# Performance work log

Hardware: AMD Instinct MI355X
Metric: run time of the kernel (lower is better)

The kernel has to match this reference:

```python
import jax, jax.numpy as jnp
import numpy as np

# Module hyperparameters (init_kwargs)
KH, KW = 1, 1            # kernel_size
PATCH_H, PATCH_W = 21, 21  # patch_size (displacement grid)
SH, SW = 1, 1            # stride
PAD_H, PAD_W = 0, 0      # padding
DILP_H, DILP_W = 1, 1    # dilation_patch
B, C, H, W = 8, 256, 64, 96


def setup_inputs() -> dict:
    key = jax.random.key(0)
    k1, k2 = jax.random.split(key)
    input1 = jax.random.normal(k1, (B, C, H, W), dtype=jnp.float32)
    input2 = jax.random.normal(k2, (B, C, H, W), dtype=jnp.float32)
    return {"input1": input1, "input2": input2}


def _correlation(x1, x2):
    """FlowNet-style spatial correlation (cost volume).

    out[b, pi, pj, i, j] = sum_{c, ki, kj}
        x1_pad[b, c, i*SH + ki, j*SW + kj] *
        x2_pad[b, c, i*SH + ki + (pi - radH)*DILP_H, j*SW + kj + (pj - radW)*DILP_W]
    Out-of-bounds reads of x2 are zero (handled by padding).
    """
    radH, radW = PATCH_H // 2, PATCH_W // 2
    x1p = jnp.pad(x1, ((0, 0), (0, 0), (PAD_H, PAD_H), (PAD_W, PAD_W)))
    x2p = jnp.pad(x2, ((0, 0), (0, 0),
                       (PAD_H + radH * DILP_H, PAD_H + radH * DILP_H),
                       (PAD_W + radW * DILP_W, PAD_W + radW * DILP_W)))
    Hp, Wp = H + 2 * PAD_H, W + 2 * PAD_W
    oH = (Hp - KH) // SH + 1
    oW = (Wp - KW) // SW + 1

    # displacement grid -> start offsets into x2p (0 corresponds to -rad shift)
    sh = jnp.arange(PATCH_H, dtype=jnp.int32) * DILP_H
    sw = jnp.arange(PATCH_W, dtype=jnp.int32) * DILP_W
    starts = jnp.stack(jnp.meshgrid(sh, sw, indexing="ij"), axis=-1).reshape(-1, 2)

    def step(carry, s):
        # shifted view of x2 aligned with padded x1
        sl = jax.lax.dynamic_slice(x2p, (0, 0, s[0], s[1]), (B, C, Hp, Wp))
        prod = jnp.sum(x1p * sl, axis=1)  # [B, Hp, Wp], channel reduction
        # kernel-window sum + output stride (KH=KW=1 -> single strided slice)
        acc = jnp.zeros((B, oH, oW), dtype=prod.dtype)
        for ki in range(KH):
            for kj in range(KW):
                acc = acc + jax.lax.slice(
                    prod, (0, ki, kj),
                    (B, ki + (oH - 1) * SH + 1, kj + (oW - 1) * SW + 1),
                    (1, SH, SW))
        return carry, acc

    _, out = jax.lax.scan(step, None, starts)  # [PATCH_H*PATCH_W, B, oH, oW]
    out = out.reshape(PATCH_H, PATCH_W, B, oH, oW)
    return jnp.transpose(out, (2, 0, 1, 3, 4))  # [B, patchH, patchW, oH, oW]


def reference(input1, input2):
    return _correlation(input1, input2)
```

## Files before the change

kernel.cpp:

```cpp
#include <hip/hip_runtime.h>

typedef __attribute__((ext_vector_type(8))) short short8;
typedef __attribute__((ext_vector_type(4))) float f32x4;
typedef __attribute__((ext_vector_type(4))) unsigned short us4;

constexpr int NB = 8, NC = 256, IH = 64, IW = 96;
constexpr int PATCH = 21, RAD = 10;
constexpr int WIN = 28;
constexpr int KC = 32, NKS = NC / KC;
constexpr int PLANE = IH * IW;
constexpr int PH = IH + 2 * RAD, PW = IW + 2 * RAD;
constexpr int NPOS = 512;
constexpr int NBCH = NPOS * 4;
constexpr int NACH = 512;
constexpr int NCHUNK = NBCH + NACH;
constexpr int ASTR = IH * IW * KC;
constexpr int BSTR = PH * PW * KC;
constexpr size_t X1T_ELEMS = (size_t)NB * NKS * ASTR;
constexpr size_t X2P_ELEMS = (size_t)NB * NKS * BSTR;
constexpr int GSTR = 129;

__device__ __forceinline__ unsigned short f2bf(float f) {
  unsigned u = __builtin_bit_cast(unsigned, f);
  u += 0x7fffu + ((u >> 16) & 1u);
  return (unsigned short)(u >> 16);
}

__global__ __launch_bounds__(256) void x1_to_kmajor(
    const float* __restrict__ src, unsigned short* __restrict__ dst) {
  __shared__ float lsf[32 * 97];
  const int blk = blockIdx.x;
  const int ct = blk & 7, i = (blk >> 3) & 63, b = blk >> 9;
  const int c0 = ct * 32, t = threadIdx.x;
  const float* sp = src + ((size_t)b * NC + c0) * PLANE + (size_t)i * IW;
#pragma unroll
  for (int k = 0; k < 12; ++k) {
    int idx = k * 256 + t;
    int c = idx / 96, j = idx - c * 96;
    lsf[c * 97 + j] = sp[(size_t)c * PLANE + j];
  }
  __syncthreads();
  unsigned short* dp = dst + (((size_t)(b * NKS + ct) * IH + i) * IW) * KC;
#pragma unroll
  for (int k = 0; k < 3; ++k) {
    int o = k * 256 + t;
    int j = o >> 3, cq = o & 7;
    us4 v = {f2bf(lsf[(cq * 4 + 0) * 97 + j]), f2bf(lsf[(cq * 4 + 1) * 97 + j]),
             f2bf(lsf[(cq * 4 + 2) * 97 + j]), f2bf(lsf[(cq * 4 + 3) * 97 + j])};
    *(us4*)&dp[(size_t)j * KC + cq * 4] = v;
  }
}

__global__ __launch_bounds__(256) void x2_to_kmajor_pad(
    const float* __restrict__ src, unsigned short* __restrict__ dst) {
  __shared__ float lsf[32 * 97];
  const int blk = blockIdx.x;
  const int ct = blk & 7, i = (blk >> 3) % PH, b = blk / (PH * 8);
  const int c0 = ct * 32, t = threadIdx.x;
  const int isrc = i - RAD;
  const bool rowok = (unsigned)isrc < (unsigned)IH;
  if (rowok) {
    const float* sp = src + ((size_t)b * NC + c0) * PLANE + (size_t)isrc * IW;
#pragma unroll
    for (int k = 0; k < 12; ++k) {
      int idx = k * 256 + t;
      int c = idx / 96, j = idx - c * 96;
      lsf[c * 97 + j] = sp[(size_t)c * PLANE + j];
    }
  }
  __syncthreads();
  unsigned short* dp = dst + (((size_t)(b * NKS + ct) * PH + i) * PW) * KC;
#pragma unroll
  for (int k = 0; k < 4; ++k) {
    int o = k * 256 + t;
    if (o < PW * 8) {
      int j = o >> 3, cq = o & 7;
      int jsrc = j - RAD;
      us4 v = {0, 0, 0, 0};
      if (rowok && (unsigned)jsrc < (unsigned)IW)
        v = us4{f2bf(lsf[(cq * 4 + 0) * 97 + jsrc]), f2bf(lsf[(cq * 4 + 1) * 97 + jsrc]),
                f2bf(lsf[(cq * 4 + 2) * 97 + jsrc]), f2bf(lsf[(cq * 4 + 3) * 97 + jsrc])};
      *(us4*)&dp[(size_t)j * KC + cq * 4] = v;
    }
  }
}

__global__ __launch_bounds__(512, 2) void corr_half(
    const unsigned short* __restrict__ x1k, const unsigned short* __restrict__ x2k,
    float* __restrict__ out) {
  __shared__ __attribute__((aligned(16))) unsigned short ls[3 * NCHUNK * 8];

  const int t = threadIdx.x, lane = t & 63, wv = t >> 6;
  const int bid = blockIdx.x;
  const int b = bid & 7;
  const int tile = bid >> 3;
  const int v = tile & 1;
  const int tt = tile >> 1;
  const int ti = tt / 12, tj = tt % 12;
  const int i0 = 16 * ti, j0 = 8 * tj;
  const int mg = wv >> 2;
  const int cg = wv & 3;
  const int cbeg = 8 * cg;
  const int qk = lane >> 4, lr = lane & 15;

  const unsigned short* x1b = x1k + (size_t)b * NKS * ASTR;
  const unsigned short* x2b = x2k + (size_t)b * NKS * BSTR;

  const unsigned short* srcp[5];
#pragma unroll
  for (int it = 0; it < 5; ++it) {
    int q = it * 512 + t;
    if (q < NBCH) {
      int w = ((q >> 3) << 1) | (((q >> 2) ^ (q >> 4)) & 1);
      int c4 = (q & 3) ^ (w & 3);
      int wd = (w >= 504) ? (w - 504) : w;
      int wi = wd / WIN, wj = wd - wi * WIN;
      srcp[it] = x2b + ((size_t)(i0 + 18 * v + wi) * PW + (j0 + wj)) * KC + c4 * 8;
    } else {
      int qa = q - NBCH;
      int m = ((qa >> 3) << 1) | (((qa >> 2) ^ (qa >> 4)) & 1);
      int c4 = (qa & 3) ^ (m & 3);
      srcp[it] = x1b + ((size_t)(i0 + (m >> 3)) * IW + (j0 + (m & 7))) * KC + c4 * 8;
    }
  }

  f32x4 acc[4][8];
#pragma unroll
  for (int a = 0; a < 4; ++a)
#pragma unroll
    for (int cc = 0; cc < 8; ++cc) acc[a][cc] = (f32x4){0.f, 0.f, 0.f, 0.f};

#define STAGE(BUF, KS)                                                              \
  {                                                                                 \
    unsigned short* lb = &ls[(BUF) * NCHUNK * 8];                                   \
    _Pragma("unroll")                                                               \
    for (int it = 0; it < 5; ++it)                                                  \
      __builtin_amdgcn_global_load_lds(                                             \
          (const void*)(srcp[it] + (size_t)(KS) * (it < 4 ? BSTR : ASTR)),          \
          (void*)(lb + (it * 512 + wv * 64) * 8), 16, 0, 0);                        \
  }

#define COMPUTE(BUF)                                                                \
  {                                                                                 \
    const unsigned short* lb = &ls[(BUF) * NCHUNK * 8];                             \
    short8 af0 = *(const short8*)(lb + (NBCH + ((64 * (4 * mg + 0) + 4 * lr + qk) ^ (lr & 7))) * 8); \
    short8 af1 = *(const short8*)(lb + (NBCH + ((64 * (4 * mg + 1) + 4 * lr + qk) ^ (lr & 7))) * 8); \
    short8 af2 = *(const short8*)(lb + (NBCH + ((64 * (4 * mg + 2) + 4 * lr + qk) ^ (lr & 7))) * 8); \
    short8 af3 = *(const short8*)(lb + (NBCH + ((64 * (4 * mg + 3) + 4 * lr + qk) ^ (lr & 7))) * 8); \
    _Pragma("unroll")                                                               \
    for (int cc = 0; cc < 8; ++cc) {                                                \
      int wrow = 16 * (cbeg + cc) + lr;                                             \
      int slot = (4 * wrow + qk) ^ (lr & 7);                                        \
      short8 bf = *(const short8*)(lb + slot * 8);                                  \
      acc[0][cc] = __builtin_amdgcn_mfma_f32_16x16x32_bf16(af0, bf, acc[0][cc], 0, 0, 0); \
      acc[1][cc] = __builtin_amdgcn_mfma_f32_16x16x32_bf16(af1, bf, acc[1][cc], 0, 0, 0); \
      acc[2][cc] = __builtin_amdgcn_mfma_f32_16x16x32_bf16(af2, bf, acc[2][cc], 0, 0, 0); \
      acc[3][cc] = __builtin_amdgcn_mfma_f32_16x16x32_bf16(af3, bf, acc[3][cc], 0, 0, 0); \
    }                                                                               \
  }

  STAGE(0, 0)
  STAGE(1, 1)

#define ITER(KS, VM)                                           \
  if ((KS) < 6) STAGE(((KS) + 2) % 3, (KS) + 2)                \
  asm volatile("s_waitcnt vmcnt(" #VM ")" ::: "memory");       \
  asm volatile("s_barrier" ::: "memory");                      \
  COMPUTE((KS) % 3)                                            \
  asm volatile("s_barrier" ::: "memory");

  ITER(0, 10)
  ITER(1, 10)
  ITER(2, 10)
  ITER(3, 10)
  ITER(4, 10)
  ITER(5, 10)
  ITER(6, 5)
  ITER(7, 0)
#undef ITER
#undef COMPUTE
#undef STAGE

  float* gf = (float*)ls;
#pragma unroll
  for (int p = 0; p < 2 + 1; ++p) {
    __syncthreads();
    const int R0 = 168 * p;
#pragma unroll
    for (int a = 0; a < 4; ++a)
#pragma unroll
      for (int cc = 0; cc < 8; ++cc) {
        int n = 16 * (cbeg + cc) + lr;
        if (n >= R0 && n < R0 + 168) {
          int rl = n - R0;
          int sm = 4 * (4 * mg + a) + qk;
          float* gp = &gf[rl * GSTR + 4 * (sm ^ (rl & 7))];
          gp[0] = acc[a][cc][0]; gp[1] = acc[a][cc][1];
          gp[2] = acc[a][cc][2]; gp[3] = acc[a][cc][3];
        }
      }
    __syncthreads();
    int segs = 0;
#pragma unroll
    for (int kk = 0; kk < 6; ++kk) {
      int W = 18 * v + 6 * p + kk;
      int hi = W < 15 ? W : 15, lo = W - 20 > 0 ? W - 20 : 0;
      segs += hi - lo + 1;
    }
    segs *= 21;
    for (int s = t; s < segs; s += 512) {
      int pidx = s / 21, pj = s - pidx * 21;
      int k = 0, rem = pidx, stop = 0;
#pragma unroll
      for (int kk = 0; kk < 5; ++kk) {
        int W = 18 * v + 6 * p + kk;
        int hi = W < 15 ? W : 15, lo = W - 20 > 0 ? W - 20 : 0;
        int c = hi - lo + 1;
        int go = (!stop) && (rem >= c);
        rem -= go ? c : 0;
        k += go;
        stop |= !go;
      }
      int W = 18 * v + 6 * p + k;
      int lo = W - 20 > 0 ? W - 20 : 0;
      int ii = lo + rem;
      int pi = W - ii;
      int rl0 = 28 * k + pj;
      float g[8];
#pragma unroll
      for (int e = 0; e < 8; ++e) {
        int m = 8 * ii + e, row = rl0 + e;
        g[e] = gf[row * GSTR + 4 * ((m >> 2) ^ (row & 7)) + (m & 3)];
      }
      float* op = out + ((((size_t)b * PATCH + pi) * PATCH + pj) * IH + (i0 + ii)) * IW + j0;
      f32x4 v0 = {g[0], g[1], g[2], g[3]};
      f32x4 v1 = {g[4], g[5], g[6], g[7]};
      *(f32x4*)op = v0;
      *(f32x4*)(op + 4) = v1;
    }
  }
}

constexpr int LDKF = 40;
constexpr int NWINF = 784;
__global__ __launch_bounds__(512, 2) void corr_mfma_fb(
    const float* __restrict__ x1, const float* __restrict__ x2, float* __restrict__ out) {
  __shared__ __attribute__((aligned(16))) unsigned short lsA[64 * LDKF];
  __shared__ __attribute__((aligned(16))) unsigned short lsB[NWINF * LDKF];
  const int t = threadIdx.x;
  const int b = blockIdx.y;
  const int ti = blockIdx.x / 12, tj = blockIdx.x % 12;
  const int i0 = ti * 8, j0 = tj * 8;
  const int lane = t & 63, wv = t >> 6;
  const int mtp = wv >> 2, cg = wv & 3, cbeg = cg * 12;
  const int qk = lane >> 4, lr = lane & 15;
  f32x4 acc[2][13];
#pragma unroll
  for (int a = 0; a < 2; ++a)
#pragma unroll
    for (int cc = 0; cc < 13; ++cc) acc[a][cc] = (f32x4){0.f, 0.f, 0.f, 0.f};
  const int am = t & 63, ak4 = t >> 6;
  const int aii = am >> 3, ajj = am & 7;
  const float* x1p = x1 + ((size_t)b * NC + 4 * ak4) * PLANE + (size_t)(i0 + aii) * IW + (j0 + ajj);
  const float* x2b = x2 + (size_t)b * NC * PLANE;
  for (int ks = 0; ks < NKS; ++ks) {
    __syncthreads();
    {
      const float* p = x1p + (size_t)ks * KC * PLANE;
      us4 v = {f2bf(p[0]), f2bf(p[PLANE]), f2bf(p[2 * PLANE]), f2bf(p[3 * PLANE])};
      *(us4*)&lsA[am * LDKF + 4 * ak4] = v;
    }
    for (int w = t; w < NWINF; w += 512) {
      const int wi = w / WIN, wj = w - wi * WIN;
      const int gi = i0 - RAD + wi, gj = j0 - RAD + wj;
      const bool ok = ((unsigned)gi < (unsigned)IH) && ((unsigned)gj < (unsigned)IW);
      const float* p = x2b + ((size_t)(ks * KC) * IH + gi) * IW + gj;
      unsigned short* dst = &lsB[w * LDKF];
#pragma unroll
      for (int k4 = 0; k4 < 8; ++k4) {
        const float* q = p + (size_t)(4 * k4) * PLANE;
        us4 v = {f2bf(ok ? q[0] : 0.f), f2bf(ok ? q[PLANE] : 0.f),
                 f2bf(ok ? q[2 * PLANE] : 0.f), f2bf(ok ? q[3 * PLANE] : 0.f)};
        *(us4*)&dst[4 * k4] = v;
      }
    }
    __syncthreads();
    short8 a0 = *(const short8*)&lsA[(32 * mtp + lr) * LDKF + 8 * qk];
    short8 a1 = *(const short8*)&lsA[(32 * mtp + 16 + lr) * LDKF + 8 * qk];
#pragma unroll
    for (int cc = 0; cc < 13; ++cc) {
      const int wrow = 16 * (cbeg + cc) + lr;
      short8 bf = *(const short8*)&lsB[wrow * LDKF + 8 * qk];
      acc[0][cc] = __builtin_amdgcn_mfma_f32_16x16x32_bf16(a0, bf, acc[0][cc], 0, 0, 0);
      acc[1][cc] = __builtin_amdgcn_mfma_f32_16x16x32_bf16(a1, bf, acc[1][cc], 0, 0, 0);
    }
  }
#pragma unroll
  for (int a = 0; a < 2; ++a) {
    const int mb = 16 * (2 * mtp + a) + qk * 4;
#pragma unroll
    for (int cc = 0; cc < 13; ++cc) {
      if (cg > 0 && cc == 0) continue;
      const int n = 16 * (cbeg + cc) + lr;
      const int wi = n / WIN, wj = n - wi * WIN;
#pragma unroll
      for (int r = 0; r < 4; ++r) {
        const int m = mb + r;
        const int ii = m >> 3, jj = m & 7;
        const int pi = wi - ii, pj = wj - jj;
        if ((unsigned)pi < (unsigned)PATCH && (unsigned)pj < (unsigned)PATCH)
          out[((((size_t)b * PATCH + pi) * PATCH + pj) * IH + (i0 + ii)) * IW + (j0 + jj)] =
              acc[a][cc][r];
      }
    }
  }
}

extern "C" void kernel_launch(void* const* d_in, const int* in_sizes, int n_in,
                              void* d_out, int out_size, void* d_ws, size_t ws_size,
                              hipStream_t stream) {
  const float* x1 = (const float*)d_in[0];
  const float* x2 = (const float*)d_in[1];
  float* out = (float*)d_out;
  const size_t need = (X1T_ELEMS + X2P_ELEMS) * sizeof(unsigned short);
  if (ws_size >= need) {
    unsigned short* x1k = (unsigned short*)d_ws;
    unsigned short* x2k = x1k + X1T_ELEMS;
    x1_to_kmajor<<<NB * IH * 8, 256, 0, stream>>>(x1, x1k);
    x2_to_kmajor_pad<<<NB * PH * 8, 256, 0, stream>>>(x2, x2k);
    corr_half<<<NB * 96, 512, 0, stream>>>(x1k, x2k, out);
  } else {
    dim3 grid(96, NB);
    corr_mfma_fb<<<grid, 512, 0, stream>>>(x1, x2, out);
  }
}
```

Measured before the change: 87.73 us.

## Merge layout prepasses into one launch and switch correlation to 32x32 MFMA

The two fp32-to-bf16 k-major conversion kernels are merged into a single launch, and their global reads are widened to float4. The main correlation kernel now uses 32x32x16 bf16 MFMA tiles instead of 16x16x32. Each wave holds 2x4 32x32 accumulators rather than the 4x8 16x16 grid, which changes the LDS fragment reads and the epilogue scatter layout. The goal is to cut launch overhead, reduce global load instructions, and raise MFMA efficiency with fewer LDS fragment loads. The cost is a different register footprint and an unswizzled epilogue write that may cause LDS bank conflicts.

```diff
diff --git a/kernel.cpp b/kernel.cpp
--- a/kernel.cpp
+++ b/kernel.cpp
@@ -2,6 +2,7 @@
 
 typedef __attribute__((ext_vector_type(8))) short short8;
 typedef __attribute__((ext_vector_type(4))) float f32x4;
+typedef __attribute__((ext_vector_type(16))) float f32x16;
 typedef __attribute__((ext_vector_type(4))) unsigned short us4;
 
 constexpr int NB = 8, NC = 256, IH = 64, IW = 96;
@@ -19,6 +20,8 @@
 constexpr size_t X1T_ELEMS = (size_t)NB * NKS * ASTR;
 constexpr size_t X2P_ELEMS = (size_t)NB * NKS * BSTR;
 constexpr int GSTR = 129;
+constexpr int X1BLKS = NB * IH * 8;
+constexpr int X2BLKS = NB * PH * 8;
 
 __device__ __forceinline__ unsigned short f2bf(float f) {
   unsigned u = __builtin_bit_cast(unsigned, f);
@@ -26,66 +29,70 @@
   return (unsigned short)(u >> 16);
 }
 
-__global__ __launch_bounds__(256) void x1_to_kmajor(
-    const float* __restrict__ src, unsigned short* __restrict__ dst) {
+__global__ __launch_bounds__(256) void prepass_kmajor(
+    const float* __restrict__ x1, const float* __restrict__ x2,
+    unsigned short* __restrict__ x1k, unsigned short* __restrict__ x2k) {
   __shared__ float lsf[32 * 97];
-  const int blk = blockIdx.x;
-  const int ct = blk & 7, i = (blk >> 3) & 63, b = blk >> 9;
-  const int c0 = ct * 32, t = threadIdx.x;
-  const float* sp = src + ((size_t)b * NC + c0) * PLANE + (size_t)i * IW;
-#pragma unroll
-  for (int k = 0; k < 12; ++k) {
-    int idx = k * 256 + t;
-    int c = idx / 96, j = idx - c * 96;
-    lsf[c * 97 + j] = sp[(size_t)c * PLANE + j];
-  }
-  __syncthreads();
-  unsigned short* dp = dst + (((size_t)(b * NKS + ct) * IH + i) * IW) * KC;
-#pragma unroll
-  for (int k = 0; k < 3; ++k) {
-    int o = k * 256 + t;
-    int j = o >> 3, cq = o & 7;
-    us4 v = {f2bf(lsf[(cq * 4 + 0) * 97 + j]), f2bf(lsf[(cq * 4 + 1) * 97 + j]),
-             f2bf(lsf[(cq * 4 + 2) * 97 + j]), f2bf(lsf[(cq * 4 + 3) * 97 + j])};
-    *(us4*)&dp[(size_t)j * KC + cq * 4] = v;
-  }
-}
-
-__global__ __launch_bounds__(256) void x2_to_kmajor_pad(
-    const float* __restrict__ src, unsigned short* __restrict__ dst) {
-  __shared__ float lsf[32 * 97];
-  const int blk = blockIdx.x;
-  const int ct = blk & 7, i = (blk >> 3) % PH, b = blk / (PH * 8);
-  const int c0 = ct * 32, t = threadIdx.x;
-  const int isrc = i - RAD;
-  const bool rowok = (unsigned)isrc < (unsigned)IH;
-  if (rowok) {
-    const float* sp = src + ((size_t)b * NC + c0) * PLANE + (size_t)isrc * IW;
-#pragma unroll
-    for (int k = 0; k < 12; ++k) {
+  const int t = threadIdx.x;
+  if (blockIdx.x < X1BLKS) {
+    const int blk = blockIdx.x;
+    const int ct = blk & 7, i = (blk >> 3) & 63, b = blk >> 9;
+    const int c0 = ct * 32;
+    const float* sp = x1 + ((size_t)b * NC + c0) * PLANE + (size_t)i * IW;
+#pragma unroll
+    for (int k = 0; k < 3; ++k) {
       int idx = k * 256 + t;
-      int c = idx / 96, j = idx - c * 96;
-      lsf[c * 97 + j] = sp[(size_t)c * PLANE + j];
-    }
-  }
-  __syncthreads();
-  unsigned short* dp = dst + (((size_t)(b * NKS + ct) * PH + i) * PW) * KC;
-#pragma unroll
-  for (int k = 0; k < 4; ++k) {
-    int o = k * 256 + t;
-    if (o < PW * 8) {
+      int c = idx / 24, j4 = idx - c * 24;
+      f32x4 v = *(const f32x4*)(sp + (size_t)c * PLANE + 4 * j4);
+      float* lp = &lsf[c * 97 + 4 * j4];
+      lp[0] = v[0]; lp[1] = v[1]; lp[2] = v[2]; lp[3] = v[3];
+    }
+    __syncthreads();
+    unsigned short* dp = x1k + (((size_t)(b * NKS + ct) * IH + i) * IW) * KC;
+#pragma unroll
+    for (int k = 0; k < 3; ++k) {
+      int o = k * 256 + t;
       int j = o >> 3, cq = o & 7;
-      int jsrc = j - RAD;
-      us4 v = {0, 0, 0, 0};
-      if (rowok && (unsigned)jsrc < (unsigned)IW)
-        v = us4{f2bf(lsf[(cq * 4 + 0) * 97 + jsrc]), f2bf(lsf[(cq * 4 + 1) * 97 + jsrc]),
-                f2bf(lsf[(cq * 4 + 2) * 97 + jsrc]), f2bf(lsf[(cq * 4 + 3) * 97 + jsrc])};
+      us4 v = {f2bf(lsf[(cq * 4 + 0) * 97 + j]), f2bf(lsf[(cq * 4 + 1) * 97 + j]),
+               f2bf(lsf[(cq * 4 + 2) * 97 + j]), f2bf(lsf[(cq * 4 + 3) * 97 + j])};
       *(us4*)&dp[(size_t)j * KC + cq * 4] = v;
     }
-  }
-}
-
-__global__ __launch_bounds__(512, 2) void corr_half(
+  } else {
+    const int blk = blockIdx.x - X1BLKS;
+    const int ct = blk & 7, i = (blk >> 3) % PH, b = blk / (PH * 8);
+    const int c0 = ct * 32;
+    const int isrc = i - RAD;
+    const bool rowok = (unsigned)isrc < (unsigned)IH;
+    if (rowok) {
+      const float* sp = x2 + ((size_t)b * NC + c0) * PLANE + (size_t)isrc * IW;
+#pragma unroll
+      for (int k = 0; k < 3; ++k) {
+        int idx = k * 256 + t;
+        int c = idx / 24, j4 = idx - c * 24;
+        f32x4 v = *(const f32x4*)(sp + (size_t)c * PLANE + 4 * j4);
+        float* lp = &lsf[c * 97 + 4 * j4];
+        lp[0] = v[0]; lp[1] = v[1]; lp[2] = v[2]; lp[3] = v[3];
+      }
+    }
+    __syncthreads();
+    unsigned short* dp = x2k + (((size_t)(b * NKS + ct) * PH + i) * PW) * KC;
+#pragma unroll
+    for (int k = 0; k < 4; ++k) {
+      int o = k * 256 + t;
+      if (o < PW * 8) {
+        int j = o >> 3, cq = o & 7;
+        int jsrc = j - RAD;
+        us4 v = {0, 0, 0, 0};
+        if (rowok && (unsigned)jsrc < (unsigned)IW)
+          v = us4{f2bf(lsf[(cq * 4 + 0) * 97 + jsrc]), f2bf(lsf[(cq * 4 + 1) * 97 + jsrc]),
+                  f2bf(lsf[(cq * 4 + 2) * 97 + jsrc]), f2bf(lsf[(cq * 4 + 3) * 97 + jsrc])};
+        *(us4*)&dp[(size_t)j * KC + cq * 4] = v;
+      }
+    }
+  }
+}
+
+__global__ __launch_bounds__(512, 2) void corr_half32(
     const unsigned short* __restrict__ x1k, const unsigned short* __restrict__ x2k,
     float* __restrict__ out) {
   __shared__ __attribute__((aligned(16))) unsigned short ls[3 * NCHUNK * 8];
@@ -98,9 +105,7 @@
   const int tt = tile >> 1;
   const int ti = tt / 12, tj = tt % 12;
   const int i0 = 16 * ti, j0 = 8 * tj;
-  const int mg = wv >> 2;
-  const int cg = wv & 3;
-  const int cbeg = 8 * cg;
+  const int l31 = lane & 31, h2 = lane >> 5;
   const int qk = lane >> 4, lr = lane & 15;
 
   const unsigned short* x1b = x1k + (size_t)b * NKS * ASTR;
@@ -123,12 +128,15 @@
       srcp[it] = x1b + ((size_t)(i0 + (m >> 3)) * IW + (j0 + (m & 7))) * KC + c4 * 8;
     }
   }
-
-  f32x4 acc[4][8];
-#pragma unroll
-  for (int a = 0; a < 4; ++a)
-#pragma unroll
-    for (int cc = 0; cc < 8; ++cc) acc[a][cc] = (f32x4){0.f, 0.f, 0.f, 0.f};
+  (void)qk; (void)lr;
+
+  f32x16 acc[2][4];
+#pragma unroll
+  for (int cc = 0; cc < 2; ++cc)
+#pragma unroll
+    for (int mt = 0; mt < 4; ++mt)
+#pragma unroll
+      for (int e = 0; e < 16; ++e) acc[cc][mt][e] = 0.f;
 
 #define STAGE(BUF, KS)                                                              \
   {                                                                                 \
@@ -143,19 +151,26 @@
 #define COMPUTE(BUF)                                                                \
   {                                                                                 \
     const unsigned short* lb = &ls[(BUF) * NCHUNK * 8];                             \
-    short8 af0 = *(const short8*)(lb + (NBCH + ((64 * (4 * mg + 0) + 4 * lr + qk) ^ (lr & 7))) * 8); \
-    short8 af1 = *(const short8*)(lb + (NBCH + ((64 * (4 * mg + 1) + 4 * lr + qk) ^ (lr & 7))) * 8); \
-    short8 af2 = *(const short8*)(lb + (NBCH + ((64 * (4 * mg + 2) + 4 * lr + qk) ^ (lr & 7))) * 8); \
-    short8 af3 = *(const short8*)(lb + (NBCH + ((64 * (4 * mg + 3) + 4 * lr + qk) ^ (lr & 7))) * 8); \
+    short8 afr[4][2];                                                               \
     _Pragma("unroll")                                                               \
-    for (int cc = 0; cc < 8; ++cc) {                                                \
-      int wrow = 16 * (cbeg + cc) + lr;                                             \
-      int slot = (4 * wrow + qk) ^ (lr & 7);                                        \
-      short8 bf = *(const short8*)(lb + slot * 8);                                  \
-      acc[0][cc] = __builtin_amdgcn_mfma_f32_16x16x32_bf16(af0, bf, acc[0][cc], 0, 0, 0); \
-      acc[1][cc] = __builtin_amdgcn_mfma_f32_16x16x32_bf16(af1, bf, acc[1][cc], 0, 0, 0); \
-      acc[2][cc] = __builtin_amdgcn_mfma_f32_16x16x32_bf16(af2, bf, acc[2][cc], 0, 0, 0); \
-      acc[3][cc] = __builtin_amdgcn_mfma_f32_16x16x32_bf16(af3, bf, acc[3][cc], 0, 0, 0); \
+    for (int mt = 0; mt < 4; ++mt)                                                  \
+      _Pragma("unroll")                                                             \
+      for (int h = 0; h < 2; ++h) {                                                 \
+        int m = 32 * mt + l31, c4q = 2 * h + h2;                                    \
+        afr[mt][h] = *(const short8*)(lb + (NBCH + ((4 * m + c4q) ^ (m & 7))) * 8); \
+      }                                                                             \
+    _Pragma("unroll")                                                               \
+    for (int cc = 0; cc < 2; ++cc) {                                                \
+      int wq = 32 * (2 * wv + cc) + l31;                                            \
+      _Pragma("unroll")                                                             \
+      for (int h = 0; h < 2; ++h) {                                                 \
+        int c4q = 2 * h + h2;                                                       \
+        short8 bf = *(const short8*)(lb + (((4 * wq + c4q) ^ (wq & 7))) * 8);       \
+        _Pragma("unroll")                                                           \
+        for (int mt = 0; mt < 4; ++mt)                                              \
+          acc[cc][mt] = __builtin_amdgcn_mfma_f32_32x32x16_bf16(afr[mt][h], bf,     \
+                                                                acc[cc][mt], 0, 0, 0); \
+      }                                                                             \
     }                                                                               \
   }
 
@@ -183,22 +198,26 @@
 
   float* gf = (float*)ls;
 #pragma unroll
-  for (int p = 0; p < 2 + 1; ++p) {
+  for (int p = 0; p < 3; ++p) {
     __syncthreads();
     const int R0 = 168 * p;
 #pragma unroll
-    for (int a = 0; a < 4; ++a)
-#pragma unroll
-      for (int cc = 0; cc < 8; ++cc) {
-        int n = 16 * (cbeg + cc) + lr;
-        if (n >= R0 && n < R0 + 168) {
-          int rl = n - R0;
-          int sm = 4 * (4 * mg + a) + qk;
-          float* gp = &gf[rl * GSTR + 4 * (sm ^ (rl & 7))];
-          gp[0] = acc[a][cc][0]; gp[1] = acc[a][cc][1];
-          gp[2] = acc[a][cc][2]; gp[3] = acc[a][cc][3];
-        }
-      }
+    for (int cc = 0; cc < 2; ++cc) {
+      int n = 32 * (2 * wv + cc) + l31;
+      if (n >= R0 && n < R0 + 168 && n < 504) {
+        float* gr = &gf[(n - R0) * GSTR];
+#pragma unroll
+        for (int mt = 0; mt < 4; ++mt)
+#pragma unroll
+          for (int q = 0; q < 4; ++q) {
+            float* gp = &gr[32 * mt + 8 * q + 4 * h2];
+            gp[0] = acc[cc][mt][4 * q + 0];
+            gp[1] = acc[cc][mt][4 * q + 1];
+            gp[2] = acc[cc][mt][4 * q + 2];
+            gp[3] = acc[cc][mt][4 * q + 3];
+          }
+      }
+    }
     __syncthreads();
     int segs = 0;
 #pragma unroll
@@ -228,10 +247,7 @@
       int rl0 = 28 * k + pj;
       float g[8];
 #pragma unroll
-      for (int e = 0; e < 8; ++e) {
-        int m = 8 * ii + e, row = rl0 + e;
-        g[e] = gf[row * GSTR + 4 * ((m >> 2) ^ (row & 7)) + (m & 3)];
-      }
+      for (int e = 0; e < 8; ++e) g[e] = gf[(rl0 + e) * GSTR + 8 * ii + e];
       float* op = out + ((((size_t)b * PATCH + pi) * PATCH + pj) * IH + (i0 + ii)) * IW + j0;
       f32x4 v0 = {g[0], g[1], g[2], g[3]};
       f32x4 v1 = {g[4], g[5], g[6], g[7]};
@@ -326,9 +342,8 @@
   if (ws_size >= need) {
     unsigned short* x1k = (unsigned short*)d_ws;
     unsigned short* x2k = x1k + X1T_ELEMS;
-    x1_to_kmajor<<<NB * IH * 8, 256, 0, stream>>>(x1, x1k);
-    x2_to_kmajor_pad<<<NB * PH * 8, 256, 0, stream>>>(x2, x2k);
-    corr_half<<<NB * 96, 512, 0, stream>>>(x1k, x2k, out);
+    prepass_kmajor<<<X1BLKS + X2BLKS, 256, 0, stream>>>(x1, x2, x1k, x2k);
+    corr_half32<<<NB * 96, 512, 0, stream>>>(x1k, x2k, out);
   } else {
     dim3 grid(96, NB);
     corr_mfma_fb<<<grid, 512, 0, stream>>>(x1, x2, out);
```

Result: faster. 82.81 us (-5.6%).
